# Kernel optimization log

Measured on AMD Instinct MI355X. Metric: run time of the kernel, lower is better.

The kernel has to match this reference:

```python
import jax, jax.numpy as jnp
import numpy as np

B, D, N = 2048, 512, 100000


def setup_inputs() -> dict:
    key = jax.random.key(0)
    k1, k2, k3 = jax.random.split(key, 3)
    queries = jax.random.normal(k1, (B, D), dtype=jnp.float32)
    X = jax.random.normal(k2, (N, D), dtype=jnp.float32)
    Y = jax.random.randint(k3, (N,), 0, 2, dtype=jnp.int64)
    return {"queries": queries, "X": X, "Y": Y, "K": 5}


def reference(queries, X, Y, K):
    # Pairwise squared Euclidean distance: ||q||^2 - 2 q.X^T + ||x||^2.
    # Use negative distance so lax.top_k returns nearest neighbors.
    q2 = jnp.sum(queries * queries, axis=1, keepdims=True)        # [B, 1]
    x2 = jnp.sum(X * X, axis=1)                                   # [N]
    neg_dist = 2.0 * (queries @ X.T) - q2 - x2[None, :]           # [B, N]
    _, idx = jax.lax.top_k(neg_dist, K)                           # [B, K]
    # Gather neighbor labels and count votes (fraction of class-1 neighbors).
    neighbor_labels = Y[idx].astype(jnp.float32)                  # [B, K]
    votes = jnp.mean(neighbor_labels, axis=1)                     # [B]
    # tf.pad(tf.expand_dims(votes, 1), [[0,0],[0,1]]) -> [B, 2]
    return jnp.pad(votes[:, None], ((0, 0), (0, 1)))
```

## Files before the change

### kernel.cpp

```cpp
#include <hip/hip_runtime.h>
#include <math.h>

typedef unsigned int   u32;
typedef unsigned short u16;
typedef short short8 __attribute__((ext_vector_type(8)));
typedef float f32x4   __attribute__((ext_vector_type(4)));
typedef float f32x16  __attribute__((ext_vector_type(16)));

constexpr int B    = 2048;
constexpr int D    = 512;
constexpr int N    = 100000;
constexpr int KTOP = 5;
constexpr int NK   = 16;

constexpr int NPART    = 48;
constexpr int CHUNK    = 2112;
constexpr int ITERS    = CHUNK / 32;
constexpr int NPTS_PAD = NPART * CHUNK;
constexpr int NPG32    = NPTS_PAD / 32;

__device__ __forceinline__ u16 f2bf(float f) {
    u32 u = __float_as_uint(f);
    return (u16)((u + 0x7fffu + ((u >> 16) & 1u)) >> 16);
}

__device__ __forceinline__ void gld_lds16(const void* g, void* l) {
    __builtin_amdgcn_global_load_lds((const __attribute__((address_space(1))) u32*)g,
                                     (__attribute__((address_space(3))) u32*)l, 16, 0, 0);
}

__device__ __forceinline__ void ins5(float (&s)[KTOP], int (&x)[KTOP], float v, int p) {
    if (v > s[KTOP - 1]) {
        s[KTOP - 1] = v; x[KTOP - 1] = p;
#pragma unroll
        for (int k = KTOP - 1; k > 0; --k) {
            if (s[k] > s[k - 1]) {
                float tf = s[k]; s[k] = s[k - 1]; s[k - 1] = tf;
                int   tg = x[k]; x[k] = x[k - 1]; x[k - 1] = tg;
            }
        }
    }
}

__device__ __forceinline__ void merge_xor(float (&s)[KTOP], int (&x)[KTOP], int mask) {
    float bs[KTOP], as[KTOP]; int bx[KTOP], ax[KTOP];
#pragma unroll
    for (int k = 0; k < KTOP; ++k) {
        bs[k] = __shfl_xor(s[k], mask); bx[k] = __shfl_xor(x[k], mask);
        as[k] = s[k]; ax[k] = x[k];
    }
#pragma unroll
    for (int k = 0; k < KTOP; ++k) {
        bool ta = (as[0] > bs[0]) || ((as[0] == bs[0]) && (ax[0] < bx[0]));
        s[k] = ta ? as[0] : bs[0];
        x[k] = ta ? ax[0] : bx[0];
#pragma unroll
        for (int m = 0; m < KTOP - 1; ++m) {
            as[m] = ta ? as[m + 1] : as[m];     ax[m] = ta ? ax[m + 1] : ax[m];
            bs[m] = ta ? bs[m]     : bs[m + 1]; bx[m] = ta ? bx[m]     : bx[m + 1];
        }
        as[KTOP - 1] = ta ? -INFINITY : as[KTOP - 1];
        bs[KTOP - 1] = ta ? bs[KTOP - 1] : -INFINITY;
    }
}

__global__ void prep_q32(const float* __restrict__ Q, u16* __restrict__ Qbf) {
    int tid  = blockIdx.x * 256 + threadIdx.x;
    int q    = tid >> 6;
    int koct = tid & 63;
    const float4* src = (const float4*)(Q + (size_t)q * D + koct * 8);
    float4 a = src[0], b = src[1];
    u32 p0 = (u32)f2bf(a.x) | ((u32)f2bf(a.y) << 16);
    u32 p1 = (u32)f2bf(a.z) | ((u32)f2bf(a.w) << 16);
    u32 p2 = (u32)f2bf(b.x) | ((u32)f2bf(b.y) << 16);
    u32 p3 = (u32)f2bf(b.z) | ((u32)f2bf(b.w) << 16);
    int kstep = koct >> 1, octet = koct & 1;
    int lane  = (q & 31) + 32 * octet;
    size_t frag = (size_t)(q >> 5) * 32 + kstep;
    *(uint4*)(Qbf + (frag * 64 + lane) * 8) = make_uint4(p0, p1, p2, p3);
}

__global__ void prep_q16(const float* __restrict__ Q, u16* __restrict__ Qbf) {
    int tid  = blockIdx.x * 256 + threadIdx.x;
    int q    = tid >> 6;
    int koct = tid & 63;
    const float4* src = (const float4*)(Q + (size_t)q * D + koct * 8);
    float4 a = src[0], b = src[1];
    u32 p0 = (u32)f2bf(a.x) | ((u32)f2bf(a.y) << 16);
    u32 p1 = (u32)f2bf(a.z) | ((u32)f2bf(a.w) << 16);
    u32 p2 = (u32)f2bf(b.x) | ((u32)f2bf(b.y) << 16);
    u32 p3 = (u32)f2bf(b.z) | ((u32)f2bf(b.w) << 16);
    int frag = (q >> 4) * NK + (koct >> 2);
    int lane = (q & 15) + 16 * (koct & 3);
    *(uint4*)(Qbf + (size_t)frag * 512 + lane * 8) = make_uint4(p0, p1, p2, p3);
}

__global__ void prep_x2(const float* __restrict__ X, u16* __restrict__ Xbf,
                        float* __restrict__ x2) {
    __shared__ float psum[4][32];
    const int t = threadIdx.x, lane = t & 63, wave = t >> 6;
    const int pg    = blockIdx.x;
    const int pt    = lane & 31, octet = lane >> 5;
    const int point = pg * 32 + pt;
    float ssum = 0.f;
#pragma unroll
    for (int u = 0; u < 8; ++u) {
        int kstep = wave * 8 + u;
        int k     = kstep * 16 + octet * 8;
        uint4 o = make_uint4(0u, 0u, 0u, 0u);
        if (point < N) {
            const float4* src = (const float4*)(X + (size_t)point * D + k);
            float4 a = src[0], b = src[1];
            ssum = fmaf(a.x, a.x, ssum); ssum = fmaf(a.y, a.y, ssum);
            ssum = fmaf(a.z, a.z, ssum); ssum = fmaf(a.w, a.w, ssum);
            ssum = fmaf(b.x, b.x, ssum); ssum = fmaf(b.y, b.y, ssum);
            ssum = fmaf(b.z, b.z, ssum); ssum = fmaf(b.w, b.w, ssum);
            o.x = (u32)f2bf(a.x) | ((u32)f2bf(a.y) << 16);
            o.y = (u32)f2bf(a.z) | ((u32)f2bf(a.w) << 16);
            o.z = (u32)f2bf(b.x) | ((u32)f2bf(b.y) << 16);
            o.w = (u32)f2bf(b.z) | ((u32)f2bf(b.w) << 16);
        }
        *(uint4*)(Xbf + (((size_t)pg * 32 + kstep) * 64 + lane) * 8) = o;
    }
    ssum += __shfl_xor(ssum, 32);
    if (octet == 0) psum[wave][pt] = ssum;
    __syncthreads();
    if (t < 32) {
        float s = psum[0][t] + psum[1][t] + psum[2][t] + psum[3][t];
        x2[pg * 32 + t] = (pg * 32 + t < N) ? s : INFINITY;
    }
}

__global__ void x2_kernel(const float* __restrict__ X, float* __restrict__ x2, int total) {
    int lane = threadIdx.x & 63;
    int wid  = (int)((blockIdx.x * blockDim.x + threadIdx.x) >> 6);
    if (wid >= total) return;
    if (wid >= N) { if (lane == 0) x2[wid] = INFINITY; return; }
    const float* row = X + (size_t)wid * D;
    float s = 0.f;
    for (int c = lane; c < D; c += 64) { float v = row[c]; s = fmaf(v, v, s); }
#pragma unroll
    for (int off = 32; off > 0; off >>= 1) s += __shfl_down(s, off);
    if (lane == 0) x2[wid] = s;
}

__launch_bounds__(256, 3)
__global__ void knn_qreg(const u16* __restrict__ Xbf, const u16* __restrict__ Qbf,
                         const float* __restrict__ x2g,
                         float* __restrict__ cand_s, int* __restrict__ cand_i) {
    __shared__ __attribute__((aligned(16))) u16 Afr[2][16 * 512];
    const int t    = threadIdx.x;
    const int lane = t & 63;
    const int wave = t >> 6;
    const int hid  = lane >> 5;
    const int col  = lane & 31;
    const int part = blockIdx.x;
    const int qb   = blockIdx.y;
    const int pg0    = part * ITERS;
    const int pstart = part * CHUNK;

    const int qg = qb * 4 + wave;
    short8 bq[32];
#pragma unroll
    for (int ks = 0; ks < 32; ++ks)
        bq[ks] = *(const short8*)(Qbf + (((size_t)qg * 32 + ks) * 64 + lane) * 8);
    asm volatile("" ::: "memory");

    float ss[KTOP]; int si[KTOP];
#pragma unroll
    for (int k = 0; k < KTOP; ++k) { ss[k] = -INFINITY; si[k] = 0x7fffffff; }

    auto issue = [&](int it, int h) {
        const size_t fb = ((size_t)(pg0 + it) * 32 + h * 16 + wave * 4) * 64;
        const u16* src = Xbf + (fb + lane) * 8;
        u16* dst = Afr[h] + ((wave * 4) * 64 + lane) * 8;
#pragma unroll
        for (int f = 0; f < 4; ++f)
            gld_lds16(src + (size_t)f * 512, dst + f * 512);
    };

    issue(0, 0);
    for (int it = 0; it < ITERS; ++it) {
        __syncthreads();
        issue(it, 1);
        f32x16 acc = (f32x16)0.f;
#pragma unroll
        for (int k = 0; k < 16; ++k) {
            short8 af = *(const short8*)&Afr[0][k * 512 + lane * 8];
            acc = __builtin_amdgcn_mfma_f32_32x32x16_bf16(af, bq[k], acc, 0, 0, 0);
        }
        __syncthreads();
        if (it + 1 < ITERS) issue(it + 1, 0);
#pragma unroll
        for (int k = 0; k < 16; ++k) {
            short8 af = *(const short8*)&Afr[1][k * 512 + lane * 8];
            acc = __builtin_amdgcn_mfma_f32_32x32x16_bf16(af, bq[16 + k], acc, 0, 0, 0);
        }
        const int PA = pstart + it * 32 + hid * 4;
        float4 xx0 = *(const float4*)(x2g + PA);
        float4 xx1 = *(const float4*)(x2g + PA + 8);
        float4 xx2 = *(const float4*)(x2g + PA + 16);
        float4 xx3 = *(const float4*)(x2g + PA + 24);
        float s0  = fmaf(2.f, acc[0],  -xx0.x), s1  = fmaf(2.f, acc[1],  -xx0.y);
        float s2  = fmaf(2.f, acc[2],  -xx0.z), s3  = fmaf(2.f, acc[3],  -xx0.w);
        float s4  = fmaf(2.f, acc[4],  -xx1.x), s5  = fmaf(2.f, acc[5],  -xx1.y);
        float s6  = fmaf(2.f, acc[6],  -xx1.z), s7  = fmaf(2.f, acc[7],  -xx1.w);
        float s8  = fmaf(2.f, acc[8],  -xx2.x), s9  = fmaf(2.f, acc[9],  -xx2.y);
        float s10 = fmaf(2.f, acc[10], -xx2.z), s11 = fmaf(2.f, acc[11], -xx2.w);
        float s12 = fmaf(2.f, acc[12], -xx3.x), s13 = fmaf(2.f, acc[13], -xx3.y);
        float s14 = fmaf(2.f, acc[14], -xx3.z), s15 = fmaf(2.f, acc[15], -xx3.w);
        float m0 = fmaxf(fmaxf(s0, s1),   fmaxf(s2, s3));
        float m1 = fmaxf(fmaxf(s4, s5),   fmaxf(s6, s7));
        float m2 = fmaxf(fmaxf(s8, s9),   fmaxf(s10, s11));
        float m3 = fmaxf(fmaxf(s12, s13), fmaxf(s14, s15));
        float mx = fmaxf(fmaxf(m0, m1), fmaxf(m2, m3));
        if (mx > ss[KTOP - 1]) {
            ins5(ss, si, s0,  PA + 0);  ins5(ss, si, s1,  PA + 1);
            ins5(ss, si, s2,  PA + 2);  ins5(ss, si, s3,  PA + 3);
            ins5(ss, si, s4,  PA + 8);  ins5(ss, si, s5,  PA + 9);
            ins5(ss, si, s6,  PA + 10); ins5(ss, si, s7,  PA + 11);
            ins5(ss, si, s8,  PA + 16); ins5(ss, si, s9,  PA + 17);
            ins5(ss, si, s10, PA + 18); ins5(ss, si, s11, PA + 19);
            ins5(ss, si, s12, PA + 24); ins5(ss, si, s13, PA + 25);
            ins5(ss, si, s14, PA + 26); ins5(ss, si, s15, PA + 27);
        }
    }

    merge_xor(ss, si, 32);
    if (hid == 0) {
        int q = qg * 32 + col;
        size_t base = ((size_t)q * NPART + part) * KTOP;
#pragma unroll
        for (int k = 0; k < KTOP; ++k) { cand_s[base + k] = ss[k]; cand_i[base + k] = si[k]; }
    }
}

__launch_bounds__(256)
__global__ void knn_conv(const float* __restrict__ X, const u16* __restrict__ Qbf,
                         const float* __restrict__ x2g,
                         float* __restrict__ cand_s, int* __restrict__ cand_i) {
    __shared__ __attribute__((aligned(16))) u16 Bfr[16 * 512];
    __shared__ __attribute__((aligned(16))) u16 Afr[4 * 512];
    __shared__ float x2s[64];
    const int t = threadIdx.x, lane = t & 63, wave = t >> 6;
    const int quad = lane >> 4, col = lane & 15;
    const int qb = blockIdx.x, part = blockIdx.y;
    const int pstart = part * 782;
    const int pend   = min(pstart + 782, N);

    float ss[4][KTOP]; int si[4][KTOP];
#pragma unroll
    for (int j = 0; j < 4; ++j)
#pragma unroll
        for (int k = 0; k < KTOP; ++k) { ss[j][k] = -INFINITY; si[j][k] = 0x7fffffff; }

    const int nsub = (pend - pstart + 63) / 64;
    for (int sbi = 0; sbi < nsub; ++sbi) {
        const int sb = pstart + sbi * 64;
        __syncthreads();
        if (t < 64) x2s[t] = (sb + t < pend) ? x2g[sb + t] : INFINITY;
        f32x4 acc[4][4];
#pragma unroll
        for (int i = 0; i < 4; ++i)
#pragma unroll
            for (int j = 0; j < 4; ++j) acc[i][j] = (f32x4)0.f;
        for (int k0i = 0; k0i < NK; ++k0i) {
            const int k0 = k0i * 32;
            __syncthreads();
            {
                int prow = sb + wave * 16 + col;
                if (prow >= pend) prow = pend - 1;
                const float4* src = (const float4*)(X + (size_t)prow * D + k0 + quad * 8);
                float4 a = src[0], b = src[1];
                u32 p0 = (u32)f2bf(a.x) | ((u32)f2bf(a.y) << 16);
                u32 p1 = (u32)f2bf(a.z) | ((u32)f2bf(a.w) << 16);
                u32 p2 = (u32)f2bf(b.x) | ((u32)f2bf(b.y) << 16);
                u32 p3 = (u32)f2bf(b.z) | ((u32)f2bf(b.w) << 16);
                *(uint4*)(Afr + wave * 512 + lane * 8) = make_uint4(p0, p1, p2, p3);
            }
#pragma unroll
            for (int j = 0; j < 4; ++j) {
                int qgrp = qb * 16 + wave * 4 + j;
                gld_lds16(Qbf + ((size_t)qgrp * NK + k0i) * 512 + lane * 8,
                          (void*)(Bfr + (wave * 4 + j) * 512));
            }
            __syncthreads();
            short8 af[4], bqf[4];
#pragma unroll
            for (int i = 0; i < 4; ++i) af[i] = *(const short8*)(Afr + i * 512 + lane * 8);
#pragma unroll
            for (int j = 0; j < 4; ++j) bqf[j] = *(const short8*)(Bfr + (wave * 4 + j) * 512 + lane * 8);
#pragma unroll
            for (int i = 0; i < 4; ++i)
#pragma unroll
                for (int j = 0; j < 4; ++j)
                    acc[i][j] = __builtin_amdgcn_mfma_f32_16x16x32_bf16(af[i], bqf[j], acc[i][j], 0, 0, 0);
        }
#pragma unroll
        for (int i = 0; i < 4; ++i) {
            int pb = 16 * i + quad * 4;
#pragma unroll
            for (int j = 0; j < 4; ++j)
#pragma unroll
                for (int r = 0; r < 4; ++r)
                    ins5(ss[j], si[j], 2.f * acc[i][j][r] - x2s[pb + r], sb + pb + r);
        }
    }
#pragma unroll
    for (int j = 0; j < 4; ++j) { merge_xor(ss[j], si[j], 16); merge_xor(ss[j], si[j], 32); }
    if (quad == 0) {
#pragma unroll
        for (int j = 0; j < 4; ++j) {
            int qg = qb * 256 + wave * 64 + j * 16 + col;
            size_t base = ((size_t)qg * 128 + part) * KTOP;
#pragma unroll
            for (int k = 0; k < KTOP; ++k) { cand_s[base + k] = ss[j][k]; cand_i[base + k] = si[j][k]; }
        }
    }
}

__launch_bounds__(256)
__global__ void finalize(const float* __restrict__ Q, const float* __restrict__ X,
                         const float* __restrict__ x2g, const int* __restrict__ Y,
                         const float* __restrict__ cand_s, const int* __restrict__ cand_i,
                         float* __restrict__ out, int npart) {
    __shared__ float scs[4][96];
    __shared__ int   sis[4][96];
    const int t = threadIdx.x, lane = t & 63, w = t >> 6;
    const int q = blockIdx.x * 4 + w;
    const int perlane = npart * KTOP / 16;

    if (lane < 16) {
        float ls[KTOP]; int li[KTOP];
#pragma unroll
        for (int k = 0; k < KTOP; ++k) { ls[k] = -INFINITY; li[k] = 0x7fffffff; }
        const float* cs = cand_s + (size_t)q * npart * KTOP + lane * perlane;
        const int*   ci = cand_i + (size_t)q * npart * KTOP + lane * perlane;
        for (int c = 0; c < perlane; ++c) {
            float s = cs[c]; int p = ci[c];
            if (s > ls[KTOP - 1] || (s == ls[KTOP - 1] && p < li[KTOP - 1])) {
                ls[KTOP - 1] = s; li[KTOP - 1] = p;
#pragma unroll
                for (int k = KTOP - 1; k > 0; --k) {
                    bool up = (ls[k] > ls[k - 1]) || (ls[k] == ls[k - 1] && li[k] < li[k - 1]);
                    if (up) {
                        float tf = ls[k]; ls[k] = ls[k - 1]; ls[k - 1] = tf;
                        int   tg = li[k]; li[k] = li[k - 1]; li[k - 1] = tg;
                    }
                }
            }
        }
#pragma unroll
        for (int k = 0; k < KTOP; ++k) { scs[w][lane * KTOP + k] = ls[k]; sis[w][lane * KTOP + k] = li[k]; }
    }
    __syncthreads();
    if (lane == 0) {
        float bs[16]; int bx[16];
#pragma unroll
        for (int m = 0; m < 16; ++m) { bs[m] = -INFINITY; bx[m] = 0x7fffffff; }
        for (int c = 0; c < 80; ++c) {
            float s = scs[w][c]; int p = sis[w][c];
            if (s > bs[15] || (s == bs[15] && p < bx[15])) {
                bs[15] = s; bx[15] = p;
#pragma unroll
                for (int m = 15; m > 0; --m) {
                    bool up = (bs[m] > bs[m - 1]) || (bs[m] == bs[m - 1] && bx[m] < bx[m - 1]);
                    if (up) {
                        float tf = bs[m]; bs[m] = bs[m - 1]; bs[m - 1] = tf;
                        int   tg = bx[m]; bx[m] = bx[m - 1]; bx[m - 1] = tg;
                    }
                }
            }
        }
#pragma unroll
        for (int m = 0; m < 16; ++m) sis[w][80 + m] = bx[m];
    }
    __syncthreads();
    const int c = lane & 15, seg = lane >> 4;
    int idx = sis[w][80 + c];
    const float4* xr = (const float4*)(X + (size_t)idx * D);
    const float4* qr = (const float4*)(Q + (size_t)q * D);
    float d = 0.f;
    for (int u = seg * 32; u < seg * 32 + 32; ++u) {
        float4 a = qr[u], b = xr[u];
        d = fmaf(a.x, b.x, d); d = fmaf(a.y, b.y, d);
        d = fmaf(a.z, b.z, d); d = fmaf(a.w, b.w, d);
    }
    d += __shfl_xor(d, 16);
    d += __shfl_xor(d, 32);
    float sc = 2.f * d - x2g[idx];
    if (seg == 0) scs[w][80 + c] = sc;
    __syncthreads();
    if (lane == 0) {
        float bs[KTOP]; int bx[KTOP];
#pragma unroll
        for (int k = 0; k < KTOP; ++k) { bs[k] = -INFINITY; bx[k] = 0x7fffffff; }
        for (int c2 = 0; c2 < 16; ++c2) {
            float s = scs[w][80 + c2]; int p = sis[w][80 + c2];
            if (s > bs[KTOP - 1] || (s == bs[KTOP - 1] && p < bx[KTOP - 1])) {
                bs[KTOP - 1] = s; bx[KTOP - 1] = p;
#pragma unroll
                for (int k = KTOP - 1; k > 0; --k) {
                    bool up = (bs[k] > bs[k - 1]) || (bs[k] == bs[k - 1] && bx[k] < bx[k - 1]);
                    if (up) {
                        float tf = bs[k]; bs[k] = bs[k - 1]; bs[k - 1] = tf;
                        int   tg = bx[k]; bx[k] = bx[k - 1]; bx[k - 1] = tg;
                    }
                }
            }
        }
        float sum = 0.f;
#pragma unroll
        for (int k = 0; k < KTOP; ++k) sum += (float)Y[bx[k]];
        out[2 * q]     = sum * 0.2f;
        out[2 * q + 1] = 0.f;
    }
}

extern "C" void kernel_launch(void* const* d_in, const int* in_sizes, int n_in,
                              void* d_out, int out_size, void* d_ws, size_t ws_size,
                              hipStream_t stream) {
    const float* Qf = (const float*)d_in[0];
    const float* Xf = (const float*)d_in[1];
    const int*   Y  = (const int*)d_in[2];
    float* out = (float*)d_out;
    char* ws = (char*)d_ws;

    constexpr size_t XBF_B  = (size_t)NPTS_PAD * D * 2;
    constexpr size_t QBF_B  = 2097152;
    constexpr size_t X2_B   = (size_t)NPTS_PAD * 4;
    constexpr size_t CAND_B = (size_t)B * NPART * KTOP * 4;
    constexpr size_t NEED   = XBF_B + QBF_B + X2_B + 2 * CAND_B;

    if (ws_size >= NEED) {
        u16*   Xbf    = (u16*)ws;
        u16*   Qbf    = (u16*)(ws + XBF_B);
        float* x2     = (float*)(ws + XBF_B + QBF_B);
        float* cand_s = (float*)(ws + XBF_B + QBF_B + X2_B);
        int*   cand_i = (int*)  (ws + XBF_B + QBF_B + X2_B + CAND_B);
        hipLaunchKernelGGL(prep_q32, dim3(512),       dim3(256), 0, stream, Qf, Qbf);
        hipLaunchKernelGGL(prep_x2,  dim3(NPG32),     dim3(256), 0, stream, Xf, Xbf, x2);
        hipLaunchKernelGGL(knn_qreg, dim3(NPART, 16), dim3(256), 0, stream, Xbf, Qbf, x2, cand_s, cand_i);
        hipLaunchKernelGGL(finalize, dim3(B / 4),     dim3(256), 0, stream, Qf, Xf, x2, Y, cand_s, cand_i, out, NPART);
    } else {
        u16*   Qbf    = (u16*)ws;
        float* x2     = (float*)(ws + 2097152);
        float* cand_s = (float*)(ws + 2497152);
        int*   cand_i = (int*)  (ws + 7740032);
        hipLaunchKernelGGL(prep_q16,  dim3(512),      dim3(256), 0, stream, Qf, Qbf);
        hipLaunchKernelGGL(x2_kernel, dim3(N / 4),    dim3(256), 0, stream, Xf, x2, N);
        hipLaunchKernelGGL(knn_conv,  dim3(8, 128),   dim3(256), 0, stream, Xf, Qbf, x2, cand_s, cand_i);
        hipLaunchKernelGGL(finalize,  dim3(B / 4),    dim3(256), 0, stream, Qf, Xf, x2, Y, cand_s, cand_i, out, 128);
    }
}
```

Before: 687.4 us.

## Deepen knn_qreg X pipeline to four-stage ring and stage x2 in LDS

The main kernel swaps its two-half double buffer for a four-slot ring of quarter-tile LDS buffers with three loads in flight. It synchronises through explicit s_waitcnt vmcnt plus s_barrier, so one barrier guards each quarter and global latency is better hidden behind MFMA work. The chunk's x2 norms are preloaded into shared memory instead of read from global memory each iteration. prep_x2 is rewritten to read whole rows coalesced, reduce norms with shuffles, and transpose through LDS into the fragment layout; the added manual vmcnt accounting is fragile.

```diff
diff --git a/kernel.cpp b/kernel.cpp
--- a/kernel.cpp
+++ b/kernel.cpp
@@ -97,37 +97,38 @@
 
 __global__ void prep_x2(const float* __restrict__ X, u16* __restrict__ Xbf,
                         float* __restrict__ x2) {
-    __shared__ float psum[4][32];
+    __shared__ __attribute__((aligned(16))) u16 Xl[32][520];
     const int t = threadIdx.x, lane = t & 63, wave = t >> 6;
-    const int pg    = blockIdx.x;
-    const int pt    = lane & 31, octet = lane >> 5;
-    const int point = pg * 32 + pt;
-    float ssum = 0.f;
-#pragma unroll
-    for (int u = 0; u < 8; ++u) {
-        int kstep = wave * 8 + u;
-        int k     = kstep * 16 + octet * 8;
-        uint4 o = make_uint4(0u, 0u, 0u, 0u);
+    const int pg = blockIdx.x;
+#pragma unroll
+    for (int i = 0; i < 8; ++i) {
+        const int p     = wave * 8 + i;
+        const int point = pg * 32 + p;
+        float4 a = make_float4(0.f, 0.f, 0.f, 0.f), b = a;
         if (point < N) {
-            const float4* src = (const float4*)(X + (size_t)point * D + k);
-            float4 a = src[0], b = src[1];
-            ssum = fmaf(a.x, a.x, ssum); ssum = fmaf(a.y, a.y, ssum);
-            ssum = fmaf(a.z, a.z, ssum); ssum = fmaf(a.w, a.w, ssum);
-            ssum = fmaf(b.x, b.x, ssum); ssum = fmaf(b.y, b.y, ssum);
-            ssum = fmaf(b.z, b.z, ssum); ssum = fmaf(b.w, b.w, ssum);
-            o.x = (u32)f2bf(a.x) | ((u32)f2bf(a.y) << 16);
-            o.y = (u32)f2bf(a.z) | ((u32)f2bf(a.w) << 16);
-            o.z = (u32)f2bf(b.x) | ((u32)f2bf(b.y) << 16);
-            o.w = (u32)f2bf(b.z) | ((u32)f2bf(b.w) << 16);
-        }
-        *(uint4*)(Xbf + (((size_t)pg * 32 + kstep) * 64 + lane) * 8) = o;
-    }
-    ssum += __shfl_xor(ssum, 32);
-    if (octet == 0) psum[wave][pt] = ssum;
+            const float4* src = (const float4*)(X + (size_t)point * D + lane * 8);
+            a = src[0]; b = src[1];
+        }
+        float s = 0.f;
+        s = fmaf(a.x, a.x, s); s = fmaf(a.y, a.y, s);
+        s = fmaf(a.z, a.z, s); s = fmaf(a.w, a.w, s);
+        s = fmaf(b.x, b.x, s); s = fmaf(b.y, b.y, s);
+        s = fmaf(b.z, b.z, s); s = fmaf(b.w, b.w, s);
+        u32 p0 = (u32)f2bf(a.x) | ((u32)f2bf(a.y) << 16);
+        u32 p1 = (u32)f2bf(a.z) | ((u32)f2bf(a.w) << 16);
+        u32 p2 = (u32)f2bf(b.x) | ((u32)f2bf(b.y) << 16);
+        u32 p3 = (u32)f2bf(b.z) | ((u32)f2bf(b.w) << 16);
+        *(uint4*)&Xl[p][lane * 8] = make_uint4(p0, p1, p2, p3);
+        s += __shfl_xor(s, 1);  s += __shfl_xor(s, 2);  s += __shfl_xor(s, 4);
+        s += __shfl_xor(s, 8);  s += __shfl_xor(s, 16); s += __shfl_xor(s, 32);
+        if (lane == 0) x2[pg * 32 + p] = (point < N) ? s : INFINITY;
+    }
     __syncthreads();
-    if (t < 32) {
-        float s = psum[0][t] + psum[1][t] + psum[2][t] + psum[3][t];
-        x2[pg * 32 + t] = (pg * 32 + t < N) ? s : INFINITY;
+#pragma unroll
+    for (int v = 0; v < 8; ++v) {
+        const int ks = v * 4 + wave;
+        uint4 o = *(const uint4*)&Xl[lane & 31][ks * 16 + (lane >> 5) * 8];
+        *(uint4*)(Xbf + (((size_t)pg * 32 + ks) * 64 + lane) * 8) = o;
     }
 }
 
@@ -148,7 +149,8 @@
 __global__ void knn_qreg(const u16* __restrict__ Xbf, const u16* __restrict__ Qbf,
                          const float* __restrict__ x2g,
                          float* __restrict__ cand_s, int* __restrict__ cand_i) {
-    __shared__ __attribute__((aligned(16))) u16 Afr[2][16 * 512];
+    __shared__ __attribute__((aligned(16))) u16 Afr[4][8 * 512];
+    __shared__ __attribute__((aligned(16))) float x2s[CHUNK];
     const int t    = threadIdx.x;
     const int lane = t & 63;
     const int wave = t >> 6;
@@ -166,41 +168,29 @@
         bq[ks] = *(const short8*)(Qbf + (((size_t)qg * 32 + ks) * 64 + lane) * 8);
     asm volatile("" ::: "memory");
 
+    for (int i = t; i < CHUNK / 4; i += 256)
+        ((float4*)x2s)[i] = ((const float4*)(x2g + pstart))[i];
+
     float ss[KTOP]; int si[KTOP];
 #pragma unroll
     for (int k = 0; k < KTOP; ++k) { ss[k] = -INFINITY; si[k] = 0x7fffffff; }
 
-    auto issue = [&](int it, int h) {
-        const size_t fb = ((size_t)(pg0 + it) * 32 + h * 16 + wave * 4) * 64;
+    auto issue = [&](int ph) {
+        const int buf = ph & 3;
+        const size_t fb = ((size_t)(pg0 + (ph >> 2)) * 32 + (ph & 3) * 8 + wave * 2) * 64;
         const u16* src = Xbf + (fb + lane) * 8;
-        u16* dst = Afr[h] + ((wave * 4) * 64 + lane) * 8;
-#pragma unroll
-        for (int f = 0; f < 4; ++f)
-            gld_lds16(src + (size_t)f * 512, dst + f * 512);
+        u16* dst = &Afr[buf][(wave * 2) * 512 + lane * 8];
+        gld_lds16(src, dst);
+        gld_lds16(src + 512, dst + 512);
     };
 
-    issue(0, 0);
-    for (int it = 0; it < ITERS; ++it) {
-        __syncthreads();
-        issue(it, 1);
-        f32x16 acc = (f32x16)0.f;
-#pragma unroll
-        for (int k = 0; k < 16; ++k) {
-            short8 af = *(const short8*)&Afr[0][k * 512 + lane * 8];
-            acc = __builtin_amdgcn_mfma_f32_32x32x16_bf16(af, bq[k], acc, 0, 0, 0);
-        }
-        __syncthreads();
-        if (it + 1 < ITERS) issue(it + 1, 0);
-#pragma unroll
-        for (int k = 0; k < 16; ++k) {
-            short8 af = *(const short8*)&Afr[1][k * 512 + lane * 8];
-            acc = __builtin_amdgcn_mfma_f32_32x32x16_bf16(af, bq[16 + k], acc, 0, 0, 0);
-        }
-        const int PA = pstart + it * 32 + hid * 4;
-        float4 xx0 = *(const float4*)(x2g + PA);
-        float4 xx1 = *(const float4*)(x2g + PA + 8);
-        float4 xx2 = *(const float4*)(x2g + PA + 16);
-        float4 xx3 = *(const float4*)(x2g + PA + 24);
+    auto epi = [&](const f32x16& acc, int it) {
+        const int base = it * 32 + hid * 4;
+        float4 xx0 = *(const float4*)&x2s[base];
+        float4 xx1 = *(const float4*)&x2s[base + 8];
+        float4 xx2 = *(const float4*)&x2s[base + 16];
+        float4 xx3 = *(const float4*)&x2s[base + 24];
+        const int PA = pstart + base;
         float s0  = fmaf(2.f, acc[0],  -xx0.x), s1  = fmaf(2.f, acc[1],  -xx0.y);
         float s2  = fmaf(2.f, acc[2],  -xx0.z), s3  = fmaf(2.f, acc[3],  -xx0.w);
         float s4  = fmaf(2.f, acc[4],  -xx1.x), s5  = fmaf(2.f, acc[5],  -xx1.y);
@@ -224,7 +214,58 @@
             ins5(ss, si, s12, PA + 24); ins5(ss, si, s13, PA + 25);
             ins5(ss, si, s14, PA + 26); ins5(ss, si, s15, PA + 27);
         }
-    }
+    };
+
+#define WBAR(NSTR) asm volatile("s_waitcnt vmcnt(" NSTR ")\n\ts_barrier" ::: "memory")
+
+    __syncthreads();
+    issue(0); issue(1); issue(2);
+
+    for (int it = 0; it < ITERS - 1; ++it) {
+        f32x16 acc = (f32x16)0.f;
+#pragma unroll
+        for (int sub = 0; sub < 4; ++sub) {
+            WBAR("4");
+            issue(it * 4 + sub + 3);
+#pragma unroll
+            for (int k = 0; k < 8; ++k) {
+                short8 af = *(const short8*)&Afr[sub][k * 512 + lane * 8];
+                acc = __builtin_amdgcn_mfma_f32_32x32x16_bf16(af, bq[sub * 8 + k], acc, 0, 0, 0);
+            }
+        }
+        epi(acc, it);
+    }
+    {
+        const int it = ITERS - 1;
+        f32x16 acc = (f32x16)0.f;
+        WBAR("4");
+        issue(it * 4 + 3);
+#pragma unroll
+        for (int k = 0; k < 8; ++k) {
+            short8 af = *(const short8*)&Afr[0][k * 512 + lane * 8];
+            acc = __builtin_amdgcn_mfma_f32_32x32x16_bf16(af, bq[k], acc, 0, 0, 0);
+        }
+        WBAR("4");
+#pragma unroll
+        for (int k = 0; k < 8; ++k) {
+            short8 af = *(const short8*)&Afr[1][k * 512 + lane * 8];
+            acc = __builtin_amdgcn_mfma_f32_32x32x16_bf16(af, bq[8 + k], acc, 0, 0, 0);
+        }
+        WBAR("2");
+#pragma unroll
+        for (int k = 0; k < 8; ++k) {
+            short8 af = *(const short8*)&Afr[2][k * 512 + lane * 8];
+            acc = __builtin_amdgcn_mfma_f32_32x32x16_bf16(af, bq[16 + k], acc, 0, 0, 0);
+        }
+        WBAR("0");
+#pragma unroll
+        for (int k = 0; k < 8; ++k) {
+            short8 af = *(const short8*)&Afr[3][k * 512 + lane * 8];
+            acc = __builtin_amdgcn_mfma_f32_32x32x16_bf16(af, bq[24 + k], acc, 0, 0, 0);
+        }
+        epi(acc, it);
+    }
+#undef WBAR
 
     merge_xor(ss, si, 32);
     if (hid == 0) {
```

Result: faster. 655.2 us (-4.7%).
